# Optimization experiments

Hardware: AMD Instinct MI355X
Metric: run time of the kernel (lower is better)

The kernel has to match this reference:

```python
import jax, jax.numpy as jnp
import numpy as np

SPIKE_DERIV_SCALE = 0.5  # self.spike_derivScale = ones * 0.5
SPIKE_DERIV_TIME = 1.0   # self.spike_derivTime = ones * 1

@jax.custom_vjp
def spike_fn(x):
    # torch forward: 0 if x < 0 else 1
    return (x >= 0).astype(x.dtype)

def _spike_fwd(x):
    return spike_fn(x), x

def _spike_bwd(x, g):
    # surrogate gradient: derivScale * exp(-|x| / derivTime)
    return (g * SPIKE_DERIV_SCALE * jnp.exp(-jnp.abs(x) / SPIKE_DERIV_TIME),)

spike_fn.defvjp(_spike_fwd, _spike_bwd)


def _alpha_kernel(W, T):
    # W: [..., B] basis weights; Tau_b = exp(b) (arange init, non-trainable)
    # returns [..., T]: sum_b (t/tau_b) * exp(-t/tau_b) * W[..., b]
    B = W.shape[-1]
    tau = jnp.exp(jnp.arange(B, dtype=W.dtype))   # [B]
    t = jnp.arange(T, dtype=W.dtype)              # [T]
    tt = t[None, :] / tau[:, None]                # [B, T]
    basis = tt * jnp.exp(-tt)
    return jnp.einsum('...b,bt->...t', W, basis)


def _causal_conv(x, kern):
    # x: [T, S], kern: [S, K]; out[t, s] = sum_j kern[s, j] * x[t-j, s]
    # (matches torch left-zero-pad + conv1d with flipped kernel)
    S, K = kern.shape
    lhs = x.T[None]                        # [1, S, T]
    rhs = jnp.flip(kern, -1)[:, None, :]   # [S, 1, K]
    out = jax.lax.conv_general_dilated(lhs, rhs, (1,), [(K - 1, 0)],
                                       feature_group_count=S)
    return out[0].T                        # [T, S]


def _forward(S_e, S_i, C_den, C_syn_e, C_syn_i, W_s_syn, W_ns_syn, Delta_ns_syn,
             W_ns_sub, V_o, Theta_s, Theta_ns, W_ns_hist, W_s_prop, W_ns_prop,
             spike_decay, T_syn, T_hist):
    sub_no = C_den.shape[0]
    dt = S_e.dtype
    B_syn = W_ns_syn.shape[1]

    # ---- synaptic alpha-basis kernels with learned (exp) delay, per subunit & E/I channel ----
    t = jnp.arange(T_syn, dtype=dt)                               # [T_syn]
    delta = jnp.exp(Delta_ns_syn)                                 # [sub, 2]
    ts = jnp.maximum(t[None, None, :] - delta[:, :, None], 0.0)   # [sub, 2, T_syn]
    tau = jnp.exp(jnp.arange(B_syn, dtype=dt))                    # [B]
    tt = ts[:, None, :, :] / tau[None, :, None, None]             # [sub, B, 2, T_syn]
    basis = tt * jnp.exp(-tt)
    syn_kern = jnp.einsum('sbct,sbc->sct', basis, W_ns_syn)       # [sub, 2, T_syn]

    in_e = S_e @ C_syn_e.T    # [T, sub] summed excitatory drive per subunit
    in_i = S_i @ C_syn_i.T    # [T, sub]
    syn_ns_in = _causal_conv(in_e, syn_kern[:, 0]) + _causal_conv(in_i, syn_kern[:, 1])
    syn_s_in = in_e * W_s_syn[:, 0] + in_i * W_s_syn[:, 1]        # [T, sub]

    # ---- spike-history & propagation kernels, reversed so index k matches
    # window index k (oldest -> newest), i.e. kern_rev[k] = kern[T_hist-1-k] ----
    hist_kern_rev = jnp.flip(_alpha_kernel(W_ns_hist, T_hist), -1)  # [sub-1, T_hist]
    prop_kern_rev = jnp.flip(_alpha_kernel(W_ns_prop, T_hist), -1)  # [sub,   T_hist]

    C_den_child = C_den[:, 1:]   # [sub, sub-1]
    C_s = C_den[1:, 1:]          # [sub-1, sub-1]

    def step(carry, inp):
        Z_buf, X_s, Y_ns = carry          # [T_hist, sub-1], [sub-1], [sub]
        syn_ns_t, syn_s_t = inp           # [sub], [sub-1]
        spike_s_last = Z_buf[-1]
        raw_ns_prop = C_den @ Y_ns                                 # [sub]
        spike_ns_prop = Z_buf @ C_den_child.T                      # [T_hist, sub]
        f_prop = jnp.einsum('ts,st->s', spike_ns_prop, prop_kern_rev)
        f_hist = jnp.einsum('ts,st->s', Z_buf, hist_kern_rev)      # [sub-1]
        X_ns_in = syn_ns_t + f_prop + raw_ns_prop + Theta_ns
        X_ns_in = X_ns_in.at[1:].add(f_hist)
        Y_new = jax.nn.sigmoid(X_ns_in) * W_ns_sub                 # [sub]
        X_s_in = (X_s * spike_decay + syn_s_t
                  + C_s @ (spike_s_last * W_s_prop) + Theta_s)     # [sub-1]
        Z_out = spike_fn(X_s_in)
        X_s_new = jnp.where(Z_out == 1, jnp.zeros_like(X_s_in), X_s_in)  # reset on spike
        Z_buf_new = jnp.concatenate([Z_buf[1:], Z_out[None]], 0)
        return (Z_buf_new, X_s_new, Y_new), (Y_new, X_s_new, Z_out)

    init = (jnp.zeros((T_hist, sub_no - 1), dt),
            jnp.zeros((sub_no - 1,), dt),
            jnp.zeros((sub_no,), dt))
    _, (Y_seq, X_seq, Z_seq) = jax.lax.scan(step, init, (syn_ns_in, syn_s_in[:, 1:]))

    final_voltage = Y_seq[:, 0] + V_o[0]
    return final_voltage, Y_seq[:, 1:], Z_seq, X_seq


def setup_inputs() -> dict:
    key = jax.random.key(0)
    ks = jax.random.split(key, 16)
    sub_no, E_no, I_no = 20, 2000, 500
    T_data, T_syn, T_hist = 10000, 200, 50
    B_syn, B_hist, B_prop = 3, 3, 3
    # binary dendritic connectivity + one-hot synapse->subunit assignment
    C_den = (jax.random.uniform(ks[0], (sub_no, sub_no)) < 0.15).astype(jnp.float32)
    C_syn_e = jax.nn.one_hot(jax.random.randint(ks[1], (E_no,), 0, sub_no), sub_no, dtype=jnp.float32).T
    C_syn_i = jax.nn.one_hot(jax.random.randint(ks[2], (I_no,), 0, sub_no), sub_no, dtype=jnp.float32).T
    S_e = (jax.random.uniform(ks[3], (T_data, E_no)) < 0.02).astype(jnp.float32)
    S_i = (jax.random.uniform(ks[4], (T_data, I_no)) < 0.02).astype(jnp.float32)
    return {
        "S_e": S_e, "S_i": S_i,
        "C_den": C_den, "C_syn_e": C_syn_e, "C_syn_i": C_syn_i,
        "W_s_syn": jax.random.normal(ks[5], (sub_no, 2)) * 0.02,
        "W_ns_syn": jax.random.normal(ks[6], (sub_no, B_syn, 2)) * 0.02,
        "Delta_ns_syn": jax.random.uniform(ks[7], (sub_no, 2)),
        "W_ns_sub": jax.random.uniform(ks[8], (sub_no,)),
        "V_o": jax.random.normal(ks[9], (1,)),
        "Theta_s": jax.random.uniform(ks[10], (sub_no - 1,)) * -0.2,
        "Theta_ns": jax.random.uniform(ks[11], (sub_no,)) * -0.2,
        "W_ns_hist": jax.random.uniform(ks[12], (sub_no - 1, B_hist)) * -0.02,
        "W_s_prop": jax.random.uniform(ks[13], (sub_no - 1,)) * 0.02,
        "W_ns_prop": jax.random.uniform(ks[14], (sub_no, B_prop)) * 0.02,
        "spike_decay": jax.random.uniform(ks[15], (sub_no - 1,)) * 0.4,
        "T_syn": T_syn, "T_hist": T_hist,
    }


def reference(S_e, S_i, C_den, C_syn_e, C_syn_i, W_s_syn, W_ns_syn, Delta_ns_syn,
              W_ns_sub, V_o, Theta_s, Theta_ns, W_ns_hist, W_s_prop, W_ns_prop,
              spike_decay, T_syn, T_hist):
    return _forward(S_e, S_i, C_den, C_syn_e, C_syn_i, W_s_syn, W_ns_syn,
                    Delta_ns_syn, W_ns_sub, V_o, Theta_s, Theta_ns, W_ns_hist,
                    W_s_prop, W_ns_prop, spike_decay, int(T_syn), int(T_hist))
```

## Files before the change

kernel.cpp:

```cpp
#include <hip/hip_runtime.h>
#include <math.h>

#define SUB 20
#define NC 19
#define TSYN 200
#define THIST 50
#define BNUM 3
#define LSEG 16
#define WARMS 32
#define WARMY 36
#define SCH 64
#define SCHP (SCH+4)
#define YLEN (LSEG+WARMY)
#define ACHP (YLEN+4)
#define WLEN (THIST+YLEN+5)
#define TKST 51
#define RT 10

__global__ void k_prep(const float* __restrict__ C_syn_e, const float* __restrict__ C_syn_i,
                       const float* __restrict__ W_ns_syn, const float* __restrict__ Delta_ns_syn,
                       const float* __restrict__ W_ns_hist, const float* __restrict__ W_ns_prop,
                       int* __restrict__ ae, int* __restrict__ ai,
                       float* __restrict__ ke, float* __restrict__ ki,
                       float* __restrict__ histk, float* __restrict__ propk,
                       int E, int I)
{
    int idx = blockIdx.x * blockDim.x + threadIdx.x;
    if (idx < E) {
        int a = 0;
        for (int s = 0; s < SUB; ++s) if (C_syn_e[(size_t)s * E + idx] != 0.f) a = s;
        ae[idx] = a;
        return;
    }
    idx -= E;
    if (idx < I) {
        int a = 0;
        for (int s = 0; s < SUB; ++s) if (C_syn_i[(size_t)s * I + idx] != 0.f) a = s;
        ai[idx] = a;
        return;
    }
    idx -= I;
    if (idx < SUB * 2 * TSYN) {
        int j   = idx % TSYN;
        int rem = idx / TSYN;
        int c2  = rem & 1;
        int s   = rem >> 1;
        float delta = expf(Delta_ns_syn[s * 2 + c2]);
        float ts = fmaxf((float)j - delta, 0.f);
        float acc = 0.f;
        for (int b = 0; b < BNUM; ++b) {
            float tau = expf((float)b);
            float tt = ts / tau;
            acc += W_ns_syn[s * 6 + b * 2 + c2] * tt * expf(-tt);
        }
        if (c2 == 0) ke[s * TSYN + j] = acc; else ki[s * TSYN + j] = acc;
        return;
    }
    idx -= SUB * 2 * TSYN;
    if (idx < NC * THIST) {
        int j = idx % THIST, c = idx / THIST;
        float acc = 0.f;
        for (int b = 0; b < BNUM; ++b) {
            float tau = expf((float)b);
            float tt = (float)j / tau;
            acc += W_ns_hist[c * 3 + b] * tt * expf(-tt);
        }
        histk[c * THIST + j] = acc;
        return;
    }
    idx -= NC * THIST;
    if (idx < SUB * THIST) {
        int j = idx % THIST, s = idx / THIST;
        float acc = 0.f;
        for (int b = 0; b < BNUM; ++b) {
            float tau = expf((float)b);
            float tt = (float)j / tau;
            acc += W_ns_prop[s * 3 + b] * tt * expf(-tt);
        }
        propk[s * THIST + j] = acc;
    }
}

__global__ __launch_bounds__(256) void k_insum(
                        const float* __restrict__ Se, const float* __restrict__ Si,
                        const int* __restrict__ ae, const int* __restrict__ ai,
                        float* __restrict__ in_eT, float* __restrict__ in_iT,
                        int T, int E, int I)
{
    __shared__ float bins[RT * SUB];
    int tid = threadIdx.x;
    int t0 = blockIdx.y * RT;
    if (t0 >= T) return;
    int nt = min(RT, T - t0);
    bool isE = (blockIdx.x == 0);
    const float* Sp = isE ? Se : Si;
    const int*   ap = isE ? ae : ai;
    float*     outp = isE ? in_eT : in_iT;
    int N = isE ? E : I;

    for (int r = tid; r < RT * SUB; r += 256) bins[r] = 0.f;
    __syncthreads();

    int N4 = N >> 2;
    for (int g = tid; g < N4; g += 256) {
        int4 a = *(const int4*)(ap + 4 * g);
        const float* p = Sp + (size_t)t0 * N + 4 * g;
        if (nt == RT) {
            float4 v[RT];
            #pragma unroll
            for (int u = 0; u < RT; ++u) v[u] = *(const float4*)(p + (size_t)u * N);
            #pragma unroll
            for (int u = 0; u < RT; ++u) {
                float* b = &bins[u * SUB];
                if (v[u].x != 0.f) atomicAdd(&b[a.x], v[u].x);
                if (v[u].y != 0.f) atomicAdd(&b[a.y], v[u].y);
                if (v[u].z != 0.f) atomicAdd(&b[a.z], v[u].z);
                if (v[u].w != 0.f) atomicAdd(&b[a.w], v[u].w);
            }
        } else {
            for (int u = 0; u < nt; ++u) {
                float4 v = *(const float4*)(p + (size_t)u * N);
                float* b = &bins[u * SUB];
                if (v.x != 0.f) atomicAdd(&b[a.x], v.x);
                if (v.y != 0.f) atomicAdd(&b[a.y], v.y);
                if (v.z != 0.f) atomicAdd(&b[a.z], v.z);
                if (v.w != 0.f) atomicAdd(&b[a.w], v.w);
            }
        }
    }
    for (int e = 4 * N4 + tid; e < N; e += 256) {
        int s = ap[e];
        for (int u = 0; u < nt; ++u) {
            float v = Sp[(size_t)(t0 + u) * N + e];
            if (v != 0.f) atomicAdd(&bins[u * SUB + s], v);
        }
    }
    __syncthreads();

    for (int r = tid; r < SUB * nt; r += 256) {
        int s = r / nt;
        int u = r - s * nt;
        outp[(size_t)s * T + t0 + u] = bins[u * SUB + s];
    }
}

__global__ __launch_bounds__(64) void k_spkconv(
                      const float* __restrict__ Theta_s, const float* __restrict__ spike_decay,
                      const float* __restrict__ C_den, const float* __restrict__ W_s_prop,
                      const float* __restrict__ W_s_syn,
                      float* __restrict__ Zout, float* __restrict__ Xout,
                      float* __restrict__ Z_T, float* __restrict__ PZ_T,
                      const float* __restrict__ in_eT, const float* __restrict__ in_iT,
                      const float* __restrict__ ke, const float* __restrict__ ki,
                      float* __restrict__ syn_nsT,
                      int T, int NB)
{
    __shared__ float S[NC * SCHP];
    __shared__ float SX[SCH * SUB];
    __shared__ unsigned ZM[SCH];
    __shared__ float PZb[LSEG * SUB];
    __shared__ float LE[570], LI[570];
    __shared__ __align__(16) float LKE[TSYN], LKI[TSYN];
    int lane = threadIdx.x;

    if (blockIdx.x >= NB) {
        int T4 = T >> 2;
        int NB2 = (T4 + 63) >> 6;
        int bid2 = blockIdx.x - NB;
        int s  = bid2 / NB2;
        int bb = bid2 - s * NB2;
        int g0 = bb << 6;
        int tbase = g0 << 2;
        const float* be = in_eT + (size_t)s * T;
        const float* bi = in_iT + (size_t)s * T;
        if (lane < 50) {
            float4 ve4 = *(const float4*)(ke + s * TSYN + 4 * lane);
            float4 vk4 = *(const float4*)(ki + s * TSYN + 4 * lane);
            *(float4*)(&LKE[4 * lane]) = ve4;
            *(float4*)(&LKI[4 * lane]) = vk4;
        }
        int wlo = tbase - 200;
        if ((T & 3) == 0) {
            float4 we[2], wi2[2];
            #pragma unroll
            for (int k = 0; k < 2; ++k) {
                int r = lane + 64 * k;
                int rc = min(r, 113);
                int gt = wlo + 4 * rc;
                int gtc = min(max(gt, 0), T - 4);
                we[k]  = *(const float4*)(be + gtc);
                wi2[k] = *(const float4*)(bi + gtc);
            }
            #pragma unroll
            for (int k = 0; k < 2; ++k) {
                int r = lane + 64 * k;
                if (r < 114) {
                    int gt = wlo + 4 * r;
                    bool in = (gt >= 0) && (gt + 4 <= T);
                    float4 ve = we[k], vi4 = wi2[k];
                    if (!in) { ve = make_float4(0.f,0.f,0.f,0.f); vi4 = ve; }
                    int b5 = 5 * r;
                    LE[b5+0]=ve.x; LE[b5+1]=ve.y; LE[b5+2]=ve.z; LE[b5+3]=ve.w;
                    LI[b5+0]=vi4.x; LI[b5+1]=vi4.y; LI[b5+2]=vi4.z; LI[b5+3]=vi4.w;
                }
            }
        } else {
            for (int r = lane; r < 114; r += 64) {
                int gt = wlo + 4 * r;
                float4 ve, vi4;
                ve.x  = (gt + 0 >= 0 && gt + 0 < T) ? be[gt + 0] : 0.f;
                ve.y  = (gt + 1 >= 0 && gt + 1 < T) ? be[gt + 1] : 0.f;
                ve.z  = (gt + 2 >= 0 && gt + 2 < T) ? be[gt + 2] : 0.f;
                ve.w  = (gt + 3 >= 0 && gt + 3 < T) ? be[gt + 3] : 0.f;
                vi4.x = (gt + 0 >= 0 && gt + 0 < T) ? bi[gt + 0] : 0.f;
                vi4.y = (gt + 1 >= 0 && gt + 1 < T) ? bi[gt + 1] : 0.f;
                vi4.z = (gt + 2 >= 0 && gt + 2 < T) ? bi[gt + 2] : 0.f;
                vi4.w = (gt + 3 >= 0 && gt + 3 < T) ? bi[gt + 3] : 0.f;
                int b5 = 5 * r;
                LE[b5+0]=ve.x; LE[b5+1]=ve.y; LE[b5+2]=ve.z; LE[b5+3]=ve.w;
                LI[b5+0]=vi4.x; LI[b5+1]=vi4.y; LI[b5+2]=vi4.z; LI[b5+3]=vi4.w;
            }
        }
        __syncthreads();
        int t4 = g0 + lane;
        if (t4 < T4) {
            int t = t4 << 2;
            int ib = t - wlo;
            #define L5(A, i) A[(i) + ((i) >> 2)]
            float ea = L5(LE, ib + 3), eb = L5(LE, ib + 2), ec = L5(LE, ib + 1), ed = L5(LE, ib);
            float ia = L5(LI, ib + 3), ib2 = L5(LI, ib + 2), ic = L5(LI, ib + 1), id = L5(LI, ib);
            float a0 = 0.f, a1 = 0.f, a2 = 0.f, a3 = 0.f;
            #pragma unroll 4
            for (int j = 0; j < TSYN; ++j) {
                float kej = LKE[j], kij = LKI[j];
                a3 = fmaf(ea, kej, a3); a3 = fmaf(ia, kij, a3);
                a2 = fmaf(eb, kej, a2); a2 = fmaf(ib2, kij, a2);
                a1 = fmaf(ec, kej, a1); a1 = fmaf(ic, kij, a1);
                a0 = fmaf(ed, kej, a0); a0 = fmaf(id, kij, a0);
                ea = eb; eb = ec; ec = ed;
                ia = ib2; ib2 = ic; ic = id;
                int i = ib - 1 - j;
                ed = L5(LE, i);
                id = L5(LI, i);
            }
            #undef L5
            *(float4*)(syn_nsT + (size_t)s * T + t) = make_float4(a0, a1, a2, a3);
        }
        return;
    }

    int c = lane;
    bool act = c < NC;
    int t0 = blockIdx.x * LSEG;
    if (t0 >= T) return;
    int t1 = min(t0 + LSEG, T);
    int tw = max(0, t0 - WARMS);

    float M[NC];
    #pragma unroll
    for (int j = 0; j < NC; ++j)
        M[j] = act ? C_den[(c + 1) * SUB + (j + 1)] * W_s_prop[j] : 0.f;
    float Cp[NC];
    #pragma unroll
    for (int j = 0; j < NC; ++j)
        Cp[j] = (lane < SUB) ? C_den[lane * SUB + (j + 1)] : 0.f;
    float theta = act ? Theta_s[c] : 0.f;
    float decay = act ? spike_decay[c] : 0.f;

    float x = 0.f;
    unsigned zlo = 0u;
    {
        int tc = tw;
        int len = t1 - tw;
        if ((T & 3) == 0) {
            int len4 = len >> 2;
            int row  = lane % NC;
            int half = lane / NC;
            bool sact = half < 2;
            int sgs = half * 6;
            const float* bpe = in_eT + (size_t)(row + 1) * T + tc;
            const float* bpi = in_iT + (size_t)(row + 1) * T + tc;
            float w0 = W_s_syn[(row + 1) * 2 + 0];
            float w1 = W_s_syn[(row + 1) * 2 + 1];
            float4 ve[6], vi6[6];
            #pragma unroll
            for (int k = 0; k < 6; ++k) {
                int gic = min(sgs + k, len4 - 1);
                ve[k]  = *(const float4*)(bpe + 4 * gic);
                vi6[k] = *(const float4*)(bpi + 4 * gic);
            }
            #pragma unroll
            for (int k = 0; k < 6; ++k) {
                int gi = sgs + k;
                if (sact && gi < len4) {
                    float4 o;
                    o.x = fmaf(ve[k].x, w0, vi6[k].x * w1);
                    o.y = fmaf(ve[k].y, w0, vi6[k].y * w1);
                    o.z = fmaf(ve[k].z, w0, vi6[k].z * w1);
                    o.w = fmaf(ve[k].w, w0, vi6[k].w * w1);
                    *(float4*)(&S[row * SCHP + 4 * gi]) = o;
                }
            }
        } else {
            for (int r = lane; r < (NC * SCH) / 4; r += 64) {
                int e = r * 4;
                int cc = e >> 6;
                int tl = e & (SCH - 1);
                if (tl < len) {
                    float w0 = W_s_syn[(cc + 1) * 2 + 0];
                    float w1 = W_s_syn[(cc + 1) * 2 + 1];
                    for (int q = 0; q < 4; ++q) {
                        float evv = in_eT[(size_t)(cc + 1) * T + tc + tl + q];
                        float ivv = in_iT[(size_t)(cc + 1) * T + tc + tl + q];
                        S[cc * SCHP + tl + q] = fmaf(evv, w0, ivv * w1);
                    }
                }
            }
        }
        __syncthreads();
        float4 cur = act ? *(float4*)(&S[c * SCHP]) : make_float4(0.f, 0.f, 0.f, 0.f);
        for (int g = 0; g < len; g += 4) {
            float4 nxt = (act && g + 4 < len) ? *(float4*)(&S[c * SCHP + g + 4]) : cur;
            #pragma unroll
            for (int q = 0; q < 4; ++q) {
                float syn = (q == 0) ? cur.x : (q == 1) ? cur.y : (q == 2) ? cur.z : cur.w;
                float P = 0.f;
                #pragma unroll
                for (int j = 0; j < NC; ++j) {
                    float b = (float)((zlo >> j) & 1u);
                    P = fmaf(b, M[j], P);
                }
                float xin = fmaf(x, decay, syn);
                xin += P;
                xin += theta;
                bool zb = xin >= 0.f;
                zlo = (unsigned)__ballot(zb);
                x = zb ? 0.f : xin;
                int tl = g + q;
                if (act) SX[tl * SUB + c] = x;
                if (lane == NC) ZM[tl] = zlo;
            }
            cur = nxt;
        }
        __syncthreads();
        int tls = t0 - tw;
        int nl  = len - tls;
        if (lane < SUB) {
            for (int tl = 0; tl < nl; ++tl) {
                unsigned m = ZM[tls + tl];
                float acc = 0.f;
                #pragma unroll
                for (int j = 0; j < NC; ++j)
                    acc = fmaf((float)((m >> j) & 1u), Cp[j], acc);
                PZb[tl * SUB + lane] = acc;
            }
        }
        __syncthreads();
        for (int r = lane; r < nl * NC; r += 64) {
            int tl = r / NC;
            int cc = r - tl * NC;
            size_t o = (size_t)(t0 + tl) * NC + cc;
            Zout[o] = (float)((ZM[tls + tl] >> cc) & 1u);
            Xout[o] = SX[(tls + tl) * SUB + cc];
        }
        for (int r = lane; r < nl * NC; r += 64) {
            int cc = r / nl;
            int tl = r - cc * nl;
            Z_T[(size_t)cc * T + (t0 + tl)] = (float)((ZM[tls + tl] >> cc) & 1u);
        }
        for (int r = lane; r < nl * SUB; r += 64) {
            int cc = r / nl;
            int tl = r - cc * nl;
            PZ_T[(size_t)cc * T + (t0 + tl)] = PZb[tl * SUB + cc];
        }
    }
}

__global__ __launch_bounds__(64) void k_yA(
                    const float* __restrict__ syn_nsT,
                    const float* __restrict__ PZ_T, const float* __restrict__ Z_T,
                    const float* __restrict__ histk, const float* __restrict__ propk,
                    const float* __restrict__ Theta_ns,
                    const float* __restrict__ C_den, const float* __restrict__ W_ns_sub,
                    const float* __restrict__ V_o,
                    float* __restrict__ Vout, float* __restrict__ Yout, int T)
{
    __shared__ float S[SUB * ACHP];
    __shared__ float PZw[SUB * WLEN];
    __shared__ float Zw[NC * WLEN];
    __shared__ float PKw[SUB * TKST];
    __shared__ float HKw[NC * TKST];
    __shared__ float SY[YLEN * SUB];
    __shared__ __align__(16) float ybc[64];
    int lane = threadIdx.x;
    int s = lane;
    bool act = s < SUB;
    int t0 = blockIdx.x * LSEG;
    if (t0 >= T) return;
    int t1 = min(t0 + LSEG, T);
    int tw = max(0, t0 - WARMY);
    int len = t1 - tw;
    int wb = tw - THIST;

    float Crow[SUB];
    #pragma unroll
    for (int j = 0; j < SUB; ++j)
        Crow[j] = act ? C_den[s * SUB + j] : 0.f;
    float wsub = act ? W_ns_sub[s] : 0.f;
    float vo = V_o[0];

    for (int r = lane; r < SUB * WLEN; r += 64) PZw[r] = 0.f;
    for (int r = lane; r < NC * WLEN; r += 64)  Zw[r] = 0.f;
    {
        bool tact = lane < SUB + NC;
        const float* kp = (lane < SUB) ? (propk + lane * THIST)
                        : tact ? (histk + (lane - SUB) * THIST) : propk;
        float* kl = (lane < SUB) ? &PKw[lane * TKST]
                  : tact ? &HKw[(lane - SUB) * TKST] : &PKw[0];
        float2 kv[THIST / 2];
        #pragma unroll
        for (int g2 = 0; g2 < THIST / 2; ++g2)
            kv[g2] = *(const float2*)(kp + 2 * g2);
        if (tact) {
            #pragma unroll
            for (int g2 = 0; g2 < THIST / 2; ++g2) {
                kl[2 * g2]     = kv[g2].x;
                kl[2 * g2 + 1] = kv[g2].y;
            }
        }
    }
    ybc[lane] = 0.f;
    __syncthreads();
    {
        int tmin = max(0, wb);
        int tmax = t1 - 2;
        if ((T & 3) == 0) {
            int ta = tmin & ~3;
            int ng4 = ((tmax - ta) >> 2) + 1;
            bool ract = lane < SUB + NC;
            const float* rowp = (lane < SUB) ? (PZ_T + (size_t)lane * T)
                              : ract ? (Z_T + (size_t)(lane - SUB) * T) : PZ_T;
            float* ldsrow = (lane < SUB) ? &PZw[lane * WLEN]
                          : ract ? &Zw[(lane - SUB) * WLEN] : &PZw[0];
            float4 vv[28];
            #pragma unroll
            for (int gi = 0; gi < 28; ++gi) {
                int gic = min(gi, ng4 - 1);
                vv[gi] = *(const float4*)(rowp + ta + 4 * gic);
            }
            if (ract) {
                #pragma unroll
                for (int gi = 0; gi < 28; ++gi) {
                    if (gi < ng4) {
                        int t = ta + 4 * gi;
                        if (t + 0 >= tmin && t + 0 <= tmax) ldsrow[t + 0 - wb] = vv[gi].x;
                        if (t + 1 >= tmin && t + 1 <= tmax) ldsrow[t + 1 - wb] = vv[gi].y;
                        if (t + 2 >= tmin && t + 2 <= tmax) ldsrow[t + 2 - wb] = vv[gi].z;
                        if (t + 3 >= tmin && t + 3 <= tmax) ldsrow[t + 3 - wb] = vv[gi].w;
                    }
                }
            }
        } else {
            int nv = tmax - tmin + 1;
            if (nv > 0) {
                for (int r = lane; r < SUB * nv; r += 64) {
                    int ss = r / nv;
                    int ti = r - ss * nv;
                    int t = tmin + ti;
                    PZw[ss * WLEN + (t - wb)] = PZ_T[(size_t)ss * T + t];
                }
                for (int r = lane; r < NC * nv; r += 64) {
                    int cc = r / nv;
                    int ti = r - cc * nv;
                    int t = tmin + ti;
                    Zw[cc * WLEN + (t - wb)] = Z_T[(size_t)cc * T + t];
                }
            }
        }
    }
    __syncthreads();

    {
        int len4 = len >> 2;
        int nwork = SUB * len4;
        for (int o4 = lane; o4 < nwork; o4 += 64) {
            int ss  = o4 % SUB;
            int tl4 = o4 / SUB;
            int tl = 4 * tl4;
            int t = tw + tl;
            float4 sy = *(const float4*)(syn_nsT + (size_t)ss * T + t);
            float th = Theta_ns[ss];
            float u0 = sy.x + th, u1 = sy.y + th, u2 = sy.z + th, u3 = sy.w + th;
            {
                const float* bp = &PZw[ss * WLEN];
                const float* pk = &PKw[ss * TKST];
                float pa = bp[tl + 52], pb = bp[tl + 51], pc = bp[tl + 50], pd = bp[tl + 49];
                for (int j = 0; j < THIST; ++j) {
                    float k = pk[j];
                    u3 = fmaf(pa, k, u3); u2 = fmaf(pb, k, u2);
                    u1 = fmaf(pc, k, u1); u0 = fmaf(pd, k, u0);
                    pa = pb; pb = pc; pc = pd;
                    pd = bp[max(0, tl + 48 - j)];
                }
            }
            if (ss >= 1) {
                const float* bz = &Zw[(ss - 1) * WLEN];
                const float* hk = &HKw[(ss - 1) * TKST];
                float pa = bz[tl + 52], pb = bz[tl + 51], pc = bz[tl + 50], pd = bz[tl + 49];
                for (int j = 0; j < THIST; ++j) {
                    float k = hk[j];
                    u3 = fmaf(pa, k, u3); u2 = fmaf(pb, k, u2);
                    u1 = fmaf(pc, k, u1); u0 = fmaf(pd, k, u0);
                    pa = pb; pb = pc; pc = pd;
                    pd = bz[max(0, tl + 48 - j)];
                }
            }
            *(float4*)(&S[ss * ACHP + tl]) = make_float4(u0, u1, u2, u3);
        }
    }
    __syncthreads();

    float4 cur = act ? *(float4*)(&S[s * ACHP]) : make_float4(0.f, 0.f, 0.f, 0.f);
    for (int g = 0; g < len; g += 4) {
        float4 nxt = (act && g + 4 < len) ? *(float4*)(&S[s * ACHP + g + 4]) : cur;
        #pragma unroll
        for (int q = 0; q < 4; ++q) {
            float a = (q == 0) ? cur.x : (q == 1) ? cur.y : (q == 2) ? cur.z : cur.w;
            __builtin_amdgcn_wave_barrier();
            float4 Y0 = *(const float4*)(&ybc[0]);
            float4 Y1 = *(const float4*)(&ybc[4]);
            float4 Y2 = *(const float4*)(&ybc[8]);
            float4 Y3 = *(const float4*)(&ybc[12]);
            float4 Y4 = *(const float4*)(&ybc[16]);
            float u0 = a, u1 = 0.f, u2 = 0.f, u3 = 0.f;
            u0 += Crow[0]  * Y0.x;  u1 += Crow[1]  * Y0.y;
            u2 += Crow[2]  * Y0.z;  u3 += Crow[3]  * Y0.w;
            u0 += Crow[4]  * Y1.x;  u1 += Crow[5]  * Y1.y;
            u2 += Crow[6]  * Y1.z;  u3 += Crow[7]  * Y1.w;
            u0 += Crow[8]  * Y2.x;  u1 += Crow[9]  * Y2.y;
            u2 += Crow[10] * Y2.z;  u3 += Crow[11] * Y2.w;
            u0 += Crow[12] * Y3.x;  u1 += Crow[13] * Y3.y;
            u2 += Crow[14] * Y3.z;  u3 += Crow[15] * Y3.w;
            u0 += Crow[16] * Y4.x;  u1 += Crow[17] * Y4.y;
            u2 += Crow[18] * Y4.z;  u3 += Crow[19] * Y4.w;
            float u = (u0 + u1) + (u2 + u3);
            float y = wsub / (1.f + __expf(-u));
            __builtin_amdgcn_wave_barrier();
            ybc[lane] = y;
            int tl = g + q;
            if (act) SY[tl * SUB + s] = y;
        }
        cur = nxt;
    }
    __syncthreads();
    for (int r = lane; r < len * SUB; r += 64) {
        int tl = r / SUB;
        int cc = r - tl * SUB;
        int tg = tw + tl;
        if (tg >= t0) {
            float y = SY[r];
            if (cc == 0) Vout[tg] = y + vo;
            else         Yout[(size_t)tg * NC + (cc - 1)] = y;
        }
    }
}

extern "C" void kernel_launch(void* const* d_in, const int* in_sizes, int n_in,
                              void* d_out, int out_size, void* d_ws, size_t ws_size,
                              hipStream_t stream)
{
    const float* S_e          = (const float*)d_in[0];
    const float* S_i          = (const float*)d_in[1];
    const float* C_den        = (const float*)d_in[2];
    const float* C_syn_e      = (const float*)d_in[3];
    const float* C_syn_i      = (const float*)d_in[4];
    const float* W_s_syn      = (const float*)d_in[5];
    const float* W_ns_syn     = (const float*)d_in[6];
    const float* Delta_ns_syn = (const float*)d_in[7];
    const float* W_ns_sub     = (const float*)d_in[8];
    const float* V_o          = (const float*)d_in[9];
    const float* Theta_s      = (const float*)d_in[10];
    const float* Theta_ns     = (const float*)d_in[11];
    const float* W_ns_hist    = (const float*)d_in[12];
    const float* W_s_prop     = (const float*)d_in[13];
    const float* W_ns_prop    = (const float*)d_in[14];
    const float* spike_decay  = (const float*)d_in[15];

    int E = in_sizes[3] / SUB;
    int I = in_sizes[4] / SUB;
    int T = in_sizes[0] / E;

    float* out  = (float*)d_out;
    float* Vout = out;
    float* Yout = out + (size_t)T;
    float* Zout = out + (size_t)T * (1 + NC);
    float* Xout = out + (size_t)T * (1 + 2*NC);

    float* w       = (float*)d_ws;
    float* in_eT   = w;  w += (size_t)SUB * T;
    float* in_iT   = w;  w += (size_t)SUB * T;
    float* syn_nsT = w;  w += (size_t)SUB * T;
    float* PZ_T    = w;  w += (size_t)SUB * T;
    float* Z_T     = w;  w += (size_t)SUB * T;
    float* ke      = w;  w += SUB * TSYN;
    float* ki      = w;  w += SUB * TSYN;
    float* histk   = w;  w += NC * THIST;
    float* propk   = w;  w += SUB * THIST;
    int*   ae      = (int*)w;
    int*   ai      = ae + E;

    int NB = (T + LSEG - 1) / LSEG;
    int T4 = T >> 2;
    int NB2 = (T4 + 63) / 64;
    int NCONV = SUB * NB2;

    int gy = (T + RT - 1) / RT;

    int nprep = E + I + SUB * 2 * TSYN + NC * THIST + SUB * THIST;
    hipLaunchKernelGGL(k_prep, dim3((nprep + 255) / 256), dim3(256), 0, stream,
                       C_syn_e, C_syn_i, W_ns_syn, Delta_ns_syn, W_ns_hist, W_ns_prop,
                       ae, ai, ke, ki, histk, propk, E, I);
    hipLaunchKernelGGL(k_insum, dim3(2, gy), dim3(256), 0, stream,
                       S_e, S_i, ae, ai, in_eT, in_iT, T, E, I);
    hipLaunchKernelGGL(k_spkconv, dim3(NB + NCONV), dim3(64), 0, stream,
                       Theta_s, spike_decay, C_den, W_s_prop, W_s_syn,
                       Zout, Xout, Z_T, PZ_T,
                       in_eT, in_iT, ke, ki, syn_nsT, T, NB);
    hipLaunchKernelGGL(k_yA, dim3(NB), dim3(64), 0, stream,
                       syn_nsT, PZ_T, Z_T, histk, propk, Theta_ns,
                       C_den, W_ns_sub, V_o, Vout, Yout, T);
}
```

Before: 75.77 us.

## Split history convolution into separate kernel and broadcast via readlane

Moves the history/propagation convolution out of k_yA into a new k_A kernel that computes the drive A_T once per timestep across many blocks, instead of recomputing it redundantly over warmup windows inside each segment block. k_yA now only loads A_T and runs the recurrent sigmoid loop. The loop broadcasts y through readlane instead of LDS with wave barriers. This adds a kernel launch and a global round trip for A_T, in exchange for less redundant work and lower LDS use in the serial kernel.

```diff
diff --git a/kernel.cpp b/kernel.cpp
--- a/kernel.cpp
+++ b/kernel.cpp
@@ -13,9 +13,12 @@
 #define SCHP (SCH+4)
 #define YLEN (LSEG+WARMY)
 #define ACHP (YLEN+4)
-#define WLEN (THIST+YLEN+5)
-#define TKST 51
 #define RT 10
+#define AWIN 385
+
+__device__ __forceinline__ float rdlane(float v, int l) {
+    return __uint_as_float((unsigned)__builtin_amdgcn_readlane(__float_as_uint(v), l));
+}
 
 __global__ void k_prep(const float* __restrict__ C_syn_e, const float* __restrict__ C_syn_i,
                        const float* __restrict__ W_ns_syn, const float* __restrict__ Delta_ns_syn,
@@ -376,22 +379,103 @@
     }
 }
 
-__global__ __launch_bounds__(64) void k_yA(
+__global__ __launch_bounds__(64) void k_A(
                     const float* __restrict__ syn_nsT,
                     const float* __restrict__ PZ_T, const float* __restrict__ Z_T,
                     const float* __restrict__ histk, const float* __restrict__ propk,
                     const float* __restrict__ Theta_ns,
+                    float* __restrict__ A_T, int T)
+{
+    __shared__ float WP[AWIN], WZ[AWIN];
+    __shared__ __align__(16) float PK2[THIST + 2], HK2[THIST + 2];
+    int lane = threadIdx.x;
+    int T4 = T >> 2;
+    int NB2 = (T4 + 63) >> 6;
+    int s  = blockIdx.x / NB2;
+    int bb = blockIdx.x - s * NB2;
+    int g0 = bb << 6;
+    int tbase = g0 << 2;
+    int wlo = tbase - 52;
+
+    if (lane < THIST) {
+        PK2[lane] = propk[s * THIST + lane];
+        HK2[lane] = (s >= 1) ? histk[(s - 1) * THIST + lane] : 0.f;
+    }
+    const float* pzr = PZ_T + (size_t)s * T;
+    const float* zr  = (s >= 1) ? (Z_T + (size_t)(s - 1) * T) : PZ_T;
+    if ((T & 3) == 0) {
+        float4 wp[2], wz[2];
+        #pragma unroll
+        for (int k = 0; k < 2; ++k) {
+            int r = lane + 64 * k;
+            int rc = min(r, 76);
+            int gt = wlo + 4 * rc;
+            int gtc = min(max(gt, 0), T - 4);
+            wp[k] = *(const float4*)(pzr + gtc);
+            wz[k] = *(const float4*)(zr + gtc);
+        }
+        #pragma unroll
+        for (int k = 0; k < 2; ++k) {
+            int r = lane + 64 * k;
+            if (r < 77) {
+                int gt = wlo + 4 * r;
+                float4 vp = wp[k], vz = wz[k];
+                if (gt < 0) { vp = make_float4(0.f,0.f,0.f,0.f); vz = vp; }
+                if (s < 1)  { vz = make_float4(0.f,0.f,0.f,0.f); }
+                int b5 = 5 * r;
+                WP[b5+0]=vp.x; WP[b5+1]=vp.y; WP[b5+2]=vp.z; WP[b5+3]=vp.w;
+                WZ[b5+0]=vz.x; WZ[b5+1]=vz.y; WZ[b5+2]=vz.z; WZ[b5+3]=vz.w;
+            }
+        }
+    } else {
+        for (int r = lane; r < 308; r += 64) {
+            int gt = wlo + r;
+            WP[r + (r >> 2)] = (gt >= 0 && gt < T) ? pzr[gt] : 0.f;
+            WZ[r + (r >> 2)] = (s >= 1 && gt >= 0 && gt < T)
+                               ? Z_T[(size_t)(s - 1) * T + gt] : 0.f;
+        }
+    }
+    __syncthreads();
+    int t4 = g0 + lane;
+    if (t4 >= T4) return;
+    int t = t4 << 2;
+    int tl = lane << 2;
+    float4 sy = *(const float4*)(syn_nsT + (size_t)s * T + t);
+    float th = Theta_ns[s];
+    float u0 = sy.x + th, u1 = sy.y + th, u2 = sy.z + th, u3 = sy.w + th;
+    #define L5(A, i) A[(i) + ((i) >> 2)]
+    {
+        float pa = L5(WP, tl + 54), pb = L5(WP, tl + 53), pc = L5(WP, tl + 52), pd = L5(WP, tl + 51);
+        for (int j = 0; j < THIST; ++j) {
+            float k = PK2[j];
+            u3 = fmaf(pa, k, u3); u2 = fmaf(pb, k, u2);
+            u1 = fmaf(pc, k, u1); u0 = fmaf(pd, k, u0);
+            pa = pb; pb = pc; pc = pd;
+            pd = L5(WP, max(0, tl + 50 - j));
+        }
+    }
+    if (s >= 1) {
+        float pa = L5(WZ, tl + 54), pb = L5(WZ, tl + 53), pc = L5(WZ, tl + 52), pd = L5(WZ, tl + 51);
+        for (int j = 0; j < THIST; ++j) {
+            float k = HK2[j];
+            u3 = fmaf(pa, k, u3); u2 = fmaf(pb, k, u2);
+            u1 = fmaf(pc, k, u1); u0 = fmaf(pd, k, u0);
+            pa = pb; pb = pc; pc = pd;
+            pd = L5(WZ, max(0, tl + 50 - j));
+        }
+    }
+    #undef L5
+    *(float4*)(A_T + (size_t)s * T + t) = make_float4(u0, u1, u2, u3);
+}
+
+__global__ __launch_bounds__(64) void k_yA(
+                    const float* __restrict__ A_T,
                     const float* __restrict__ C_den, const float* __restrict__ W_ns_sub,
                     const float* __restrict__ V_o,
                     float* __restrict__ Vout, float* __restrict__ Yout, int T)
 {
     __shared__ float S[SUB * ACHP];
-    __shared__ float PZw[SUB * WLEN];
-    __shared__ float Zw[NC * WLEN];
-    __shared__ float PKw[SUB * TKST];
-    __shared__ float HKw[NC * TKST];
     __shared__ float SY[YLEN * SUB];
-    __shared__ __align__(16) float ybc[64];
     int lane = threadIdx.x;
     int s = lane;
     bool act = s < SUB;
@@ -400,7 +484,6 @@
     int t1 = min(t0 + LSEG, T);
     int tw = max(0, t0 - WARMY);
     int len = t1 - tw;
-    int wb = tw - THIST;
 
     float Crow[SUB];
     #pragma unroll
@@ -409,144 +492,53 @@
     float wsub = act ? W_ns_sub[s] : 0.f;
     float vo = V_o[0];
 
-    for (int r = lane; r < SUB * WLEN; r += 64) PZw[r] = 0.f;
-    for (int r = lane; r < NC * WLEN; r += 64)  Zw[r] = 0.f;
-    {
-        bool tact = lane < SUB + NC;
-        const float* kp = (lane < SUB) ? (propk + lane * THIST)
-                        : tact ? (histk + (lane - SUB) * THIST) : propk;
-        float* kl = (lane < SUB) ? &PKw[lane * TKST]
-                  : tact ? &HKw[(lane - SUB) * TKST] : &PKw[0];
-        float2 kv[THIST / 2];
+    if ((T & 3) == 0) {
+        int len4 = len >> 2;
+        int row = lane / 3;
+        int ch  = lane - row * 3;
+        bool ract = lane < SUB * 3;
+        const float* ap2 = A_T + (size_t)(ract ? row : 0) * T + tw;
+        float4 av[5];
         #pragma unroll
-        for (int g2 = 0; g2 < THIST / 2; ++g2)
-            kv[g2] = *(const float2*)(kp + 2 * g2);
-        if (tact) {
-            #pragma unroll
-            for (int g2 = 0; g2 < THIST / 2; ++g2) {
-                kl[2 * g2]     = kv[g2].x;
-                kl[2 * g2 + 1] = kv[g2].y;
-            }
-        }
-    }
-    ybc[lane] = 0.f;
+        for (int g = 0; g < 5; ++g) {
+            int gic = min(ch * 5 + g, len4 - 1);
+            av[g] = *(const float4*)(ap2 + 4 * gic);
+        }
+        if (ract) {
+            #pragma unroll
+            for (int g = 0; g < 5; ++g) {
+                int gi = ch * 5 + g;
+                if (gi < len4) *(float4*)(&S[row * ACHP + 4 * gi]) = av[g];
+            }
+        }
+    } else {
+        for (int r = lane; r < SUB * len; r += 64) {
+            int ss = r / len, tt = r - ss * len;
+            S[ss * ACHP + tt] = A_T[(size_t)ss * T + tw + tt];
+        }
+    }
     __syncthreads();
-    {
-        int tmin = max(0, wb);
-        int tmax = t1 - 2;
-        if ((T & 3) == 0) {
-            int ta = tmin & ~3;
-            int ng4 = ((tmax - ta) >> 2) + 1;
-            bool ract = lane < SUB + NC;
-            const float* rowp = (lane < SUB) ? (PZ_T + (size_t)lane * T)
-                              : ract ? (Z_T + (size_t)(lane - SUB) * T) : PZ_T;
-            float* ldsrow = (lane < SUB) ? &PZw[lane * WLEN]
-                          : ract ? &Zw[(lane - SUB) * WLEN] : &PZw[0];
-            float4 vv[28];
-            #pragma unroll
-            for (int gi = 0; gi < 28; ++gi) {
-                int gic = min(gi, ng4 - 1);
-                vv[gi] = *(const float4*)(rowp + ta + 4 * gic);
-            }
-            if (ract) {
-                #pragma unroll
-                for (int gi = 0; gi < 28; ++gi) {
-                    if (gi < ng4) {
-                        int t = ta + 4 * gi;
-                        if (t + 0 >= tmin && t + 0 <= tmax) ldsrow[t + 0 - wb] = vv[gi].x;
-                        if (t + 1 >= tmin && t + 1 <= tmax) ldsrow[t + 1 - wb] = vv[gi].y;
-                        if (t + 2 >= tmin && t + 2 <= tmax) ldsrow[t + 2 - wb] = vv[gi].z;
-                        if (t + 3 >= tmin && t + 3 <= tmax) ldsrow[t + 3 - wb] = vv[gi].w;
-                    }
-                }
-            }
-        } else {
-            int nv = tmax - tmin + 1;
-            if (nv > 0) {
-                for (int r = lane; r < SUB * nv; r += 64) {
-                    int ss = r / nv;
-                    int ti = r - ss * nv;
-                    int t = tmin + ti;
-                    PZw[ss * WLEN + (t - wb)] = PZ_T[(size_t)ss * T + t];
-                }
-                for (int r = lane; r < NC * nv; r += 64) {
-                    int cc = r / nv;
-                    int ti = r - cc * nv;
-                    int t = tmin + ti;
-                    Zw[cc * WLEN + (t - wb)] = Z_T[(size_t)cc * T + t];
-                }
-            }
-        }
-    }
-    __syncthreads();
-
-    {
-        int len4 = len >> 2;
-        int nwork = SUB * len4;
-        for (int o4 = lane; o4 < nwork; o4 += 64) {
-            int ss  = o4 % SUB;
-            int tl4 = o4 / SUB;
-            int tl = 4 * tl4;
-            int t = tw + tl;
-            float4 sy = *(const float4*)(syn_nsT + (size_t)ss * T + t);
-            float th = Theta_ns[ss];
-            float u0 = sy.x + th, u1 = sy.y + th, u2 = sy.z + th, u3 = sy.w + th;
-            {
-                const float* bp = &PZw[ss * WLEN];
-                const float* pk = &PKw[ss * TKST];
-                float pa = bp[tl + 52], pb = bp[tl + 51], pc = bp[tl + 50], pd = bp[tl + 49];
-                for (int j = 0; j < THIST; ++j) {
-                    float k = pk[j];
-                    u3 = fmaf(pa, k, u3); u2 = fmaf(pb, k, u2);
-                    u1 = fmaf(pc, k, u1); u0 = fmaf(pd, k, u0);
-                    pa = pb; pb = pc; pc = pd;
-                    pd = bp[max(0, tl + 48 - j)];
-                }
-            }
-            if (ss >= 1) {
-                const float* bz = &Zw[(ss - 1) * WLEN];
-                const float* hk = &HKw[(ss - 1) * TKST];
-                float pa = bz[tl + 52], pb = bz[tl + 51], pc = bz[tl + 50], pd = bz[tl + 49];
-                for (int j = 0; j < THIST; ++j) {
-                    float k = hk[j];
-                    u3 = fmaf(pa, k, u3); u2 = fmaf(pb, k, u2);
-                    u1 = fmaf(pc, k, u1); u0 = fmaf(pd, k, u0);
-                    pa = pb; pb = pc; pc = pd;
-                    pd = bz[max(0, tl + 48 - j)];
-                }
-            }
-            *(float4*)(&S[ss * ACHP + tl]) = make_float4(u0, u1, u2, u3);
-        }
-    }
-    __syncthreads();
-
+
+    float y = 0.f;
     float4 cur = act ? *(float4*)(&S[s * ACHP]) : make_float4(0.f, 0.f, 0.f, 0.f);
     for (int g = 0; g < len; g += 4) {
         float4 nxt = (act && g + 4 < len) ? *(float4*)(&S[s * ACHP + g + 4]) : cur;
         #pragma unroll
         for (int q = 0; q < 4; ++q) {
             float a = (q == 0) ? cur.x : (q == 1) ? cur.y : (q == 2) ? cur.z : cur.w;
-            __builtin_amdgcn_wave_barrier();
-            float4 Y0 = *(const float4*)(&ybc[0]);
-            float4 Y1 = *(const float4*)(&ybc[4]);
-            float4 Y2 = *(const float4*)(&ybc[8]);
-            float4 Y3 = *(const float4*)(&ybc[12]);
-            float4 Y4 = *(const float4*)(&ybc[16]);
             float u0 = a, u1 = 0.f, u2 = 0.f, u3 = 0.f;
-            u0 += Crow[0]  * Y0.x;  u1 += Crow[1]  * Y0.y;
-            u2 += Crow[2]  * Y0.z;  u3 += Crow[3]  * Y0.w;
-            u0 += Crow[4]  * Y1.x;  u1 += Crow[5]  * Y1.y;
-            u2 += Crow[6]  * Y1.z;  u3 += Crow[7]  * Y1.w;
-            u0 += Crow[8]  * Y2.x;  u1 += Crow[9]  * Y2.y;
-            u2 += Crow[10] * Y2.z;  u3 += Crow[11] * Y2.w;
-            u0 += Crow[12] * Y3.x;  u1 += Crow[13] * Y3.y;
-            u2 += Crow[14] * Y3.z;  u3 += Crow[15] * Y3.w;
-            u0 += Crow[16] * Y4.x;  u1 += Crow[17] * Y4.y;
-            u2 += Crow[18] * Y4.z;  u3 += Crow[19] * Y4.w;
+            u0 += Crow[0]  * rdlane(y, 0);   u1 += Crow[1]  * rdlane(y, 1);
+            u2 += Crow[2]  * rdlane(y, 2);   u3 += Crow[3]  * rdlane(y, 3);
+            u0 += Crow[4]  * rdlane(y, 4);   u1 += Crow[5]  * rdlane(y, 5);
+            u2 += Crow[6]  * rdlane(y, 6);   u3 += Crow[7]  * rdlane(y, 7);
+            u0 += Crow[8]  * rdlane(y, 8);   u1 += Crow[9]  * rdlane(y, 9);
+            u2 += Crow[10] * rdlane(y, 10);  u3 += Crow[11] * rdlane(y, 11);
+            u0 += Crow[12] * rdlane(y, 12);  u1 += Crow[13] * rdlane(y, 13);
+            u2 += Crow[14] * rdlane(y, 14);  u3 += Crow[15] * rdlane(y, 15);
+            u0 += Crow[16] * rdlane(y, 16);  u1 += Crow[17] * rdlane(y, 17);
+            u2 += Crow[18] * rdlane(y, 18);  u3 += Crow[19] * rdlane(y, 19);
             float u = (u0 + u1) + (u2 + u3);
-            float y = wsub / (1.f + __expf(-u));
-            __builtin_amdgcn_wave_barrier();
-            ybc[lane] = y;
+            y = wsub / (1.f + __expf(-u));
             int tl = g + q;
             if (act) SY[tl * SUB + s] = y;
         }
@@ -558,9 +550,9 @@
         int cc = r - tl * SUB;
         int tg = tw + tl;
         if (tg >= t0) {
-            float y = SY[r];
-            if (cc == 0) Vout[tg] = y + vo;
-            else         Yout[(size_t)tg * NC + (cc - 1)] = y;
+            float y2 = SY[r];
+            if (cc == 0) Vout[tg] = y2 + vo;
+            else         Yout[(size_t)tg * NC + (cc - 1)] = y2;
         }
     }
 }
@@ -602,6 +594,7 @@
     float* syn_nsT = w;  w += (size_t)SUB * T;
     float* PZ_T    = w;  w += (size_t)SUB * T;
     float* Z_T     = w;  w += (size_t)SUB * T;
+    float* A_T     = w;  w += (size_t)SUB * T;
     float* ke      = w;  w += SUB * TSYN;
     float* ki      = w;  w += SUB * TSYN;
     float* histk   = w;  w += NC * THIST;
@@ -626,7 +619,8 @@
                        Theta_s, spike_decay, C_den, W_s_prop, W_s_syn,
                        Zout, Xout, Z_T, PZ_T,
                        in_eT, in_iT, ke, ki, syn_nsT, T, NB);
+    hipLaunchKernelGGL(k_A, dim3(SUB * NB2), dim3(64), 0, stream,
+                       syn_nsT, PZ_T, Z_T, histk, propk, Theta_ns, A_T, T);
     hipLaunchKernelGGL(k_yA, dim3(NB), dim3(64), 0, stream,
-                       syn_nsT, PZ_T, Z_T, histk, propk, Theta_ns,
-                       C_den, W_ns_sub, V_o, Vout, Yout, T);
+                       A_T, C_den, W_ns_sub, V_o, Vout, Yout, T);
 }
```

Measured after the change: 69.23 us (median of 2 runs). 1.09x faster.
